# Kernel tuning notes

Measured on AMD Instinct MI355X. Metric: run time of the kernel, lower is better.

## Reference

```python
import jax, jax.numpy as jnp
import numpy as np

B, IN_CH, OUT_CH = 4, 64, 128
N_HIGH, N_LOW = 163842, 40962
GROUPS, EPS, SLOPE = 4, 1e-5, 0.2


def setup_inputs() -> dict:
    key = jax.random.key(0)
    ks = jax.random.split(key, 6)
    x = jax.random.normal(ks[0], (B, IN_CH, N_HIGH), jnp.float32)
    pool_neigh = jax.random.randint(ks[1], (N_LOW * 7,), 0, N_HIGH, dtype=jnp.int32)
    conv_neigh = jax.random.randint(ks[2], (N_LOW * 7,), 0, N_LOW, dtype=jnp.int32)
    W1 = jax.random.normal(ks[3], (OUT_CH, 7 * IN_CH), jnp.float32) / np.float32(np.sqrt(7 * IN_CH))
    b1 = jnp.zeros((OUT_CH,), jnp.float32)
    W2 = jax.random.normal(ks[4], (OUT_CH, 7 * OUT_CH), jnp.float32) / np.float32(np.sqrt(7 * OUT_CH))
    b2 = jnp.zeros((OUT_CH,), jnp.float32)
    return dict(x=x, pool_neigh=pool_neigh, conv_neigh=conv_neigh,
                W1=W1, b1=b1, gn1_w=jnp.ones((OUT_CH,), jnp.float32), gn1_b=jnp.zeros((OUT_CH,), jnp.float32),
                W2=W2, b2=b2, gn2_w=jnp.ones((OUT_CH,), jnp.float32), gn2_b=jnp.zeros((OUT_CH,), jnp.float32))


def _mean_pool(x, pool_neigh):
    # x: (B, C, N_high); pool_neigh: (N_low*7,) -> (B, C, N_low)
    g = x[:, :, pool_neigh].reshape(x.shape[0], x.shape[1], -1, 7)
    return g.mean(axis=-1)


def _onering_conv(x, neigh, W, b):
    # x: (B, C, N); neigh: (N*7,); W: (O, 7*C). Torch Linear over gathered
    # (N*7, C).view(N, 7*C): neighbor-major, channel-minor concatenation.
    Bb, C, N = x.shape
    feat = x[:, :, neigh].reshape(Bb, C, N, 7)            # (B, C, N, 7)
    feat = jnp.transpose(feat, (0, 2, 3, 1)).reshape(Bb, N, 7 * C)  # (B, N, 7C)
    out = jnp.einsum('bnf,of->bno', feat, W) + b          # (B, N, O)
    return jnp.transpose(out, (0, 2, 1))                  # (B, O, N)


def _group_norm(x, w, b):
    # x: (B, C, N), normalize per (group, sample) over (C//G, N)
    Bb, C, N = x.shape
    xg = x.reshape(Bb, GROUPS, C // GROUPS, N)
    mu = xg.mean(axis=(2, 3), keepdims=True)
    var = ((xg - mu) ** 2).mean(axis=(2, 3), keepdims=True)
    xn = ((xg - mu) * jax.lax.rsqrt(var + EPS)).reshape(Bb, C, N)
    return xn * w[None, :, None] + b[None, :, None]


def _leaky_relu(x):
    return jnp.where(x >= 0, x, SLOPE * x)


def reference(x, pool_neigh, conv_neigh, W1, b1, gn1_w, gn1_b, W2, b2, gn2_w, gn2_b):
    h = _mean_pool(x, pool_neigh)
    h = _leaky_relu(_group_norm(_onering_conv(h, conv_neigh, W1, b1), gn1_w, gn1_b))
    h = _leaky_relu(_group_norm(_onering_conv(h, conv_neigh, W2, b2), gn2_w, gn2_b))
    return h
```

## Files before the change

### kernel.cpp

```cpp
#include <hip/hip_runtime.h>

#define B_SZ 4
#define IN_CH 64
#define OUT_CH 128
#define NHI 163842
#define NLO 40962
#define EPS_GN 1e-5f
#define SLOPE 0.2f

typedef __attribute__((ext_vector_type(8))) short short8;
typedef __attribute__((ext_vector_type(16))) float f32x16;

__device__ inline ushort f2bf(float f) {
    union { float f; unsigned u; } v; v.f = f;
    unsigned r = v.u + 0x7FFF + ((v.u >> 16) & 1);
    return (ushort)(r >> 16);
}
__device__ inline float bf2f(ushort h) {
    union { unsigned u; float f; } v; v.u = ((unsigned)h) << 16;
    return v.f;
}

__device__ inline void glds16(const ushort* g, ushort* l) {
    typedef __attribute__((address_space(1))) const void gv;
    typedef __attribute__((address_space(3))) void lv;
    __builtin_amdgcn_global_load_lds((gv*)g, (lv*)l, 16, 0, 0);
}

__global__ void k_transpose_x(const float* __restrict__ x, ushort* __restrict__ xT) {
    __shared__ float t[64][65];
    const int b   = blockIdx.y;
    const int n0  = blockIdx.x * 64;
    const int tid = threadIdx.x;
    const int nq  = tid & 15;
    const int c0  = tid >> 4;
    const bool full = (n0 + 64) <= NHI;
    if (full) {
#pragma unroll
        for (int r = 0; r < 4; ++r) {
            int c = c0 + r * 16;
            float4 v = *(const float4*)&x[((long)b * IN_CH + c) * NHI + n0 + nq * 4];
            t[c][nq * 4 + 0] = v.x; t[c][nq * 4 + 1] = v.y;
            t[c][nq * 4 + 2] = v.z; t[c][nq * 4 + 3] = v.w;
        }
    } else {
        for (int r = 0; r < 4; ++r) {
            int c = c0 + r * 16;
            for (int e = 0; e < 4; ++e) {
                int n = n0 + nq * 4 + e;
                t[c][nq * 4 + e] = (n < NHI) ? x[((long)b * IN_CH + c) * NHI + n] : 0.f;
            }
        }
    }
    __syncthreads();
    const int n  = tid >> 2;
    const int cc = (tid & 3) * 16;
    if (n0 + n < NHI) {
        short8 o0, o1;
#pragma unroll
        for (int e = 0; e < 8; ++e) {
            o0[e] = (short)f2bf(t[cc + e][n]);
            o1[e] = (short)f2bf(t[cc + 8 + e][n]);
        }
        ushort* p = &xT[((long)b * NHI + n0 + n) * 64 + cc];
        *(short8*)p = o0;
        *(short8*)(p + 8) = o1;
    }
}

__global__ void k_prep_w(const float* __restrict__ W, ushort* __restrict__ Wb, int K) {
    int i = blockIdx.x * 256 + threadIdx.x;
    if (i >= K * 128) return;
    int k = i / 128, o = i % 128;
    int step = k >> 6, kk = k & 63, kg = kk >> 3, e = kk & 7;
    Wb[(((long)(step * 8 + kg) * 128 + o) * 8) + e] = f2bf(W[(long)o * K + k]);
}

__global__ void k_pool(const ushort* __restrict__ xT, const int* __restrict__ pn,
                       ushort* __restrict__ h1) {
    long t = (long)blockIdx.x * 256 + threadIdx.x;
    const long total = (long)B_SZ * NLO * 8;
    if (t >= total) return;
    int  cq = (int)(t & 7);
    long bn = t >> 3;
    int  n  = (int)(bn % NLO);
    int  b  = (int)(bn / NLO);
    float acc[8] = {};
#pragma unroll
    for (int j = 0; j < 7; ++j) {
        int idx = pn[n * 7 + j];
        short8 v = *(const short8*)&xT[((long)b * NHI + idx) * 64 + cq * 8];
#pragma unroll
        for (int e = 0; e < 8; ++e) acc[e] += bf2f((ushort)v[e]);
    }
    short8 o;
#pragma unroll
    for (int e = 0; e < 8; ++e) o[e] = (short)f2bf(acc[e] * (1.f / 7.f));
    *(short8*)&h1[bn * 64 + cq * 8] = o;
}

template <int CIN>
__global__ __launch_bounds__(256, 2)
void k_conv_mfma(const ushort* __restrict__ src, const int* __restrict__ nbr,
                 const ushort* __restrict__ Wb, const float* __restrict__ bias,
                 ushort* __restrict__ out, float* __restrict__ part) {
    constexpr int NSTEP = 7 * CIN / 64;
    __shared__ ushort Bsm[2][8192];
    __shared__ float  red[4][4][2];

    const int b     = blockIdx.y;
    const int n0    = blockIdx.x * 256;
    const int tid   = threadIdx.x;
    const int lane  = tid & 63;
    const int wid   = tid >> 6;
    const int l31   = lane & 31;
    const int khalf = lane >> 5;

    const int rr0 = min(n0 + wid * 64 + l31, NLO - 1);
    const int rr1 = min(n0 + wid * 64 + 32 + l31, NLO - 1);
    int nb0[7], nb1[7];
#pragma unroll
    for (int j = 0; j < 7; ++j) {
        nb0[j] = nbr[rr0 * 7 + j];
        nb1[j] = nbr[rr1 * 7 + j];
    }

    const long srcb = (long)b * NLO * CIN;
    const int  koff = khalf * 8;

    f32x16 acc[2][4] = {};
    short8 a[2][4], an[2][4];

#pragma unroll
    for (int i = 0; i < 4; ++i) {
        int off = (wid * 4 + i) * 512;
        glds16(&Wb[off + lane * 8], &Bsm[0][off]);
    }
    {
        const ushort* s0 = &src[srcb + (long)nb0[0] * CIN + koff];
        const ushort* s1 = &src[srcb + (long)nb1[0] * CIN + koff];
#pragma unroll
        for (int kh = 0; kh < 4; ++kh) {
            a[0][kh] = *(const short8*)(s0 + kh * 16);
            a[1][kh] = *(const short8*)(s1 + kh * 16);
        }
    }

#pragma unroll
    for (int step = 0; step < NSTEP; ++step) {
        const int cur = step & 1;
        __syncthreads();
        if (step + 1 < NSTEP) {
#pragma unroll
            for (int i = 0; i < 4; ++i) {
                int off = (wid * 4 + i) * 512;
                glds16(&Wb[(long)(step + 1) * 8192 + off + lane * 8], &Bsm[cur ^ 1][off]);
            }
            const int j2 = (CIN == 64) ? (step + 1) : ((step + 1) >> 1);
            const int cb2 = (CIN == 64) ? 0 : (((step + 1) & 1) * 64);
            const ushort* s0 = &src[srcb + (long)nb0[j2] * CIN + cb2 + koff];
            const ushort* s1 = &src[srcb + (long)nb1[j2] * CIN + cb2 + koff];
#pragma unroll
            for (int kh = 0; kh < 4; ++kh) {
                an[0][kh] = *(const short8*)(s0 + kh * 16);
                an[1][kh] = *(const short8*)(s1 + kh * 16);
            }
        }
#pragma unroll
        for (int kh = 0; kh < 4; ++kh) {
            const int kg = 2 * kh + khalf;
            const ushort* bb = &Bsm[cur][(kg * 128 + l31) * 8];
            short8 b0 = *(const short8*)(bb);
            short8 b1 = *(const short8*)(bb + 32 * 8);
            short8 b2 = *(const short8*)(bb + 64 * 8);
            short8 b3 = *(const short8*)(bb + 96 * 8);
            acc[0][0] = __builtin_amdgcn_mfma_f32_32x32x16_bf16(a[0][kh], b0, acc[0][0], 0, 0, 0);
            acc[0][1] = __builtin_amdgcn_mfma_f32_32x32x16_bf16(a[0][kh], b1, acc[0][1], 0, 0, 0);
            acc[0][2] = __builtin_amdgcn_mfma_f32_32x32x16_bf16(a[0][kh], b2, acc[0][2], 0, 0, 0);
            acc[0][3] = __builtin_amdgcn_mfma_f32_32x32x16_bf16(a[0][kh], b3, acc[0][3], 0, 0, 0);
            acc[1][0] = __builtin_amdgcn_mfma_f32_32x32x16_bf16(a[1][kh], b0, acc[1][0], 0, 0, 0);
            acc[1][1] = __builtin_amdgcn_mfma_f32_32x32x16_bf16(a[1][kh], b1, acc[1][1], 0, 0, 0);
            acc[1][2] = __builtin_amdgcn_mfma_f32_32x32x16_bf16(a[1][kh], b2, acc[1][2], 0, 0, 0);
            acc[1][3] = __builtin_amdgcn_mfma_f32_32x32x16_bf16(a[1][kh], b3, acc[1][3], 0, 0, 0);
        }
        if (step + 1 < NSTEP) {
#pragma unroll
            for (int kh = 0; kh < 4; ++kh) {
                a[0][kh] = an[0][kh];
                a[1][kh] = an[1][kh];
            }
        }
    }

    float bia[4];
#pragma unroll
    for (int n = 0; n < 4; ++n) bia[n] = bias[n * 32 + l31];
    float s[4] = {}, q[4] = {};
#pragma unroll
    for (int m = 0; m < 2; ++m)
#pragma unroll
        for (int n = 0; n < 4; ++n)
#pragma unroll
            for (int r = 0; r < 16; ++r) {
                int crow = (r & 3) + 8 * (r >> 2) + 4 * khalf;
                int row  = n0 + wid * 64 + m * 32 + crow;
                float v  = acc[m][n][r] + bia[n];
                if (row < NLO) {
                    out[((long)b * NLO + row) * 128 + n * 32 + l31] = f2bf(v);
                    s[n] += v; q[n] += v * v;
                }
            }
#pragma unroll
    for (int n = 0; n < 4; ++n)
#pragma unroll
        for (int off = 32; off > 0; off >>= 1) {
            s[n] += __shfl_down(s[n], off);
            q[n] += __shfl_down(q[n], off);
        }
    if (lane == 0) {
#pragma unroll
        for (int n = 0; n < 4; ++n) { red[wid][n][0] = s[n]; red[wid][n][1] = q[n]; }
    }
    __syncthreads();
    if (tid < 8) {
        int g = tid >> 1, isq = tid & 1;
        float v = red[0][g][isq] + red[1][g][isq] + red[2][g][isq] + red[3][g][isq];
        part[(((long)b * gridDim.x + blockIdx.x) * 4 + g) * 2 + isq] = v;
    }
}

__global__ void k_finalize(const float* __restrict__ part, int nblk,
                           const float* __restrict__ w, const float* __restrict__ bb,
                           float* __restrict__ scale, float* __restrict__ shift) {
    const int b = blockIdx.x >> 2, g = blockIdx.x & 3;
    const int tid = threadIdx.x;
    float s = 0.f, ss = 0.f;
    for (int k = tid; k < nblk; k += 256) {
        s  += part[(((long)b * nblk + k) * 4 + g) * 2 + 0];
        ss += part[(((long)b * nblk + k) * 4 + g) * 2 + 1];
    }
#pragma unroll
    for (int off = 32; off > 0; off >>= 1) {
        s += __shfl_down(s, off); ss += __shfl_down(ss, off);
    }
    __shared__ float red[8];
    __shared__ float fin[2];
    const int wave = tid >> 6, lane = tid & 63;
    if (lane == 0) { red[wave * 2] = s; red[wave * 2 + 1] = ss; }
    __syncthreads();
    if (tid == 0) {
        float as = red[0] + red[2] + red[4] + red[6];
        float aq = red[1] + red[3] + red[5] + red[7];
        const float cnt = 32.f * NLO;
        float mu  = as / cnt;
        float var = aq / cnt - mu * mu;
        fin[0] = mu; fin[1] = rsqrtf(var + EPS_GN);
    }
    __syncthreads();
    if (tid < 32) {
        int c = g * 32 + tid;
        float sc = fin[1] * w[c];
        scale[b * 128 + c] = sc;
        shift[b * 128 + c] = bb[c] - fin[0] * sc;
    }
}

__global__ void k_gnapply(const ushort* __restrict__ y, const float* __restrict__ sc,
                          const float* __restrict__ sh, ushort* __restrict__ yp) {
    long t = (long)blockIdx.x * 256 + threadIdx.x;
    const long total = (long)B_SZ * NLO * 16;
    if (t >= total) return;
    int  c8 = (int)(t & 15);
    long bn = t >> 4;
    int  b  = (int)(bn / NLO);
    short8 v = *(const short8*)&y[bn * 128 + c8 * 8];
    short8 o;
#pragma unroll
    for (int e = 0; e < 8; ++e) {
        int c = c8 * 8 + e;
        float f = bf2f((ushort)v[e]) * sc[b * 128 + c] + sh[b * 128 + c];
        f = fmaxf(f, SLOPE * f);
        o[e] = (short)f2bf(f);
    }
    *(short8*)&yp[bn * 128 + c8 * 8] = o;
}

__global__ void k_output(const ushort* __restrict__ y2, const float* __restrict__ scale,
                         const float* __restrict__ shift, float* __restrict__ out) {
    __shared__ float t[32][129];
    const int b   = blockIdx.y;
    const int n0  = blockIdx.x * 32;
    const int tid = threadIdx.x;
    const float* scb = &scale[b * 128];
    const float* shb = &shift[b * 128];
    const int c8 = (tid & 15) * 8;
#pragma unroll
    for (int r = 0; r < 2; ++r) {
        int nn = (tid >> 4) + r * 16;
        int n  = n0 + nn;
        if (n < NLO) {
            short8 v = *(const short8*)&y2[((long)b * NLO + n) * 128 + c8];
#pragma unroll
            for (int e = 0; e < 8; ++e) {
                int c = c8 + e;
                float f = bf2f((ushort)v[e]) * scb[c] + shb[c];
                t[nn][c] = fmaxf(f, SLOPE * f);
            }
        } else {
#pragma unroll
            for (int e = 0; e < 8; ++e) t[nn][c8 + e] = 0.f;
        }
    }
    __syncthreads();
    const int n4 = (tid & 7) * 4;
    const bool full = (n0 + 32) <= NLO;
#pragma unroll
    for (int r = 0; r < 4; ++r) {
        int c = (tid >> 3) + r * 32;
        long o = ((long)b * 128 + c) * NLO + n0 + n4;
        if (full) {
            float2 v0 = make_float2(t[n4][c], t[n4 + 1][c]);
            float2 v1 = make_float2(t[n4 + 2][c], t[n4 + 3][c]);
            *(float2*)&out[o]     = v0;
            *(float2*)&out[o + 2] = v1;
        } else {
            for (int e = 0; e < 4; ++e)
                if (n0 + n4 + e < NLO) out[o + e] = t[n4 + e][c];
        }
    }
}

extern "C" void kernel_launch(void* const* d_in, const int* in_sizes, int n_in,
                              void* d_out, int out_size, void* d_ws, size_t ws_size,
                              hipStream_t stream) {
    const float* x   = (const float*)d_in[0];
    const int*   pn  = (const int*)d_in[1];
    const int*   cn  = (const int*)d_in[2];
    const float* W1  = (const float*)d_in[3];
    const float* b1  = (const float*)d_in[4];
    const float* g1w = (const float*)d_in[5];
    const float* g1b = (const float*)d_in[6];
    const float* W2  = (const float*)d_in[7];
    const float* b2  = (const float*)d_in[8];
    const float* g2w = (const float*)d_in[9];
    const float* g2b = (const float*)d_in[10];
    float* out = (float*)d_out;
    char*  base = (char*)d_ws;

    ushort* xT  = (ushort*)(base + 0);
    ushort* y1  = (ushort*)(base + 0);
    ushort* y1p = (ushort*)(base + 44000000);
    ushort* h1  = (ushort*)(base + 88000000);
    ushort* y2  = (ushort*)(base + 110000000);
    ushort* wb1 = (ushort*)(base + 152000000);
    ushort* wb2 = (ushort*)(base + 152200000);
    float*  p1  = (float*)(base + 152500000);
    float*  p2  = (float*)(base + 152600000);
    float*  sc1 = (float*)(base + 152700000);
    float*  sh1 = sc1 + 512;
    float*  sc2 = (float*)(base + 152710000);
    float*  sh2 = sc2 + 512;

    const int NBLK = (NLO + 255) / 256;

    k_transpose_x<<<dim3((NHI + 63) / 64, B_SZ), 256, 0, stream>>>(x, xT);
    k_prep_w<<<(448 * 128 + 255) / 256, 256, 0, stream>>>(W1, wb1, 448);
    k_prep_w<<<(896 * 128 + 255) / 256, 256, 0, stream>>>(W2, wb2, 896);
    k_pool<<<(int)(((long)B_SZ * NLO * 8 + 255) / 256), 256, 0, stream>>>(xT, pn, h1);
    k_conv_mfma<64><<<dim3(NBLK, B_SZ), 256, 0, stream>>>(h1, cn, wb1, b1, y1, p1);
    k_finalize<<<16, 256, 0, stream>>>(p1, NBLK, g1w, g1b, sc1, sh1);
    k_gnapply<<<(int)(((long)B_SZ * NLO * 16 + 255) / 256), 256, 0, stream>>>(y1, sc1, sh1, y1p);
    k_conv_mfma<128><<<dim3(NBLK, B_SZ), 256, 0, stream>>>(y1p, cn, wb2, b2, y2, p2);
    k_finalize<<<16, 256, 0, stream>>>(p2, NBLK, g2w, g2b, sc2, sh2);
    k_output<<<dim3((NLO + 31) / 32, B_SZ), 256, 0, stream>>>(y2, sc2, sh2, out);
}
```

Before: 272.0 us.

## Retile conv MFMA kernel to 128-row blocks with LDS-staged gathered A tile

The one-ring conv kernel now processes 128 rows per block instead of 256, with the four waves arranged as a 2x2 grid over rows and output channels. The gathered neighbor features are loaded cooperatively and stored into a double-buffered LDS A tile before the MFMAs, instead of each wave loading its own rows straight into registers. This aims to make the gathers more contiguous, cut per-wave accumulator and register pressure, and double the number of blocks. In exchange it adds LDS write and read traffic, more LDS use per block, and a barrier every step. The GroupNorm partial-sum reduction is remapped to the new wave layout.

```diff
diff --git a/kernel.cpp b/kernel.cpp
--- a/kernel.cpp
+++ b/kernel.cpp
@@ -105,113 +105,109 @@
                  const ushort* __restrict__ Wb, const float* __restrict__ bias,
                  ushort* __restrict__ out, float* __restrict__ part) {
     constexpr int NSTEP = 7 * CIN / 64;
+    __shared__ ushort Asm[2][8192];
     __shared__ ushort Bsm[2][8192];
-    __shared__ float  red[4][4][2];
+    __shared__ float  red[4][2][2];
 
     const int b     = blockIdx.y;
-    const int n0    = blockIdx.x * 256;
+    const int n0    = blockIdx.x * 128;
     const int tid   = threadIdx.x;
     const int lane  = tid & 63;
-    const int wid   = tid >> 6;
+    const int wave  = tid >> 6;
+    const int wr    = wave >> 1, wc = wave & 1;
     const int l31   = lane & 31;
     const int khalf = lane >> 5;
 
-    const int rr0 = min(n0 + wid * 64 + l31, NLO - 1);
-    const int rr1 = min(n0 + wid * 64 + 32 + l31, NLO - 1);
+    const int s_nn = tid >> 2;
+    const int s_kq = tid & 3;
+    const int r0 = min(n0 + s_nn, NLO - 1);
+    const int r1 = min(n0 + 64 + s_nn, NLO - 1);
     int nb0[7], nb1[7];
 #pragma unroll
     for (int j = 0; j < 7; ++j) {
-        nb0[j] = nbr[rr0 * 7 + j];
-        nb1[j] = nbr[rr1 * 7 + j];
+        nb0[j] = nbr[r0 * 7 + j];
+        nb1[j] = nbr[r1 * 7 + j];
     }
 
     const long srcb = (long)b * NLO * CIN;
-    const int  koff = khalf * 8;
-
-    f32x16 acc[2][4] = {};
-    short8 a[2][4], an[2][4];
+    f32x16 acc[2][2] = {};
+    short8 a00, a01, a10, a11;
 
 #pragma unroll
     for (int i = 0; i < 4; ++i) {
-        int off = (wid * 4 + i) * 512;
+        int off = (wave * 4 + i) * 512;
         glds16(&Wb[off + lane * 8], &Bsm[0][off]);
     }
     {
-        const ushort* s0 = &src[srcb + (long)nb0[0] * CIN + koff];
-        const ushort* s1 = &src[srcb + (long)nb1[0] * CIN + koff];
-#pragma unroll
-        for (int kh = 0; kh < 4; ++kh) {
-            a[0][kh] = *(const short8*)(s0 + kh * 16);
-            a[1][kh] = *(const short8*)(s1 + kh * 16);
-        }
-    }
-
-#pragma unroll
+        const ushort* p0 = &src[srcb + (long)nb0[0] * CIN + s_kq * 8];
+        const ushort* p1 = &src[srcb + (long)nb1[0] * CIN + s_kq * 8];
+        a00 = *(const short8*)p0; a01 = *(const short8*)(p0 + 32);
+        a10 = *(const short8*)p1; a11 = *(const short8*)(p1 + 32);
+        *(short8*)&Asm[0][(s_kq * 128 + s_nn) * 8]            = a00;
+        *(short8*)&Asm[0][((s_kq + 4) * 128 + s_nn) * 8]      = a01;
+        *(short8*)&Asm[0][(s_kq * 128 + 64 + s_nn) * 8]       = a10;
+        *(short8*)&Asm[0][((s_kq + 4) * 128 + 64 + s_nn) * 8] = a11;
+    }
+    __syncthreads();
+
     for (int step = 0; step < NSTEP; ++step) {
         const int cur = step & 1;
-        __syncthreads();
+        const int nxt = cur ^ 1;
         if (step + 1 < NSTEP) {
 #pragma unroll
             for (int i = 0; i < 4; ++i) {
-                int off = (wid * 4 + i) * 512;
-                glds16(&Wb[(long)(step + 1) * 8192 + off + lane * 8], &Bsm[cur ^ 1][off]);
+                int off = (wave * 4 + i) * 512;
+                glds16(&Wb[(long)(step + 1) * 8192 + off + lane * 8], &Bsm[nxt][off]);
             }
-            const int j2 = (CIN == 64) ? (step + 1) : ((step + 1) >> 1);
-            const int cb2 = (CIN == 64) ? 0 : (((step + 1) & 1) * 64);
-            const ushort* s0 = &src[srcb + (long)nb0[j2] * CIN + cb2 + koff];
-            const ushort* s1 = &src[srcb + (long)nb1[j2] * CIN + cb2 + koff];
-#pragma unroll
-            for (int kh = 0; kh < 4; ++kh) {
-                an[0][kh] = *(const short8*)(s0 + kh * 16);
-                an[1][kh] = *(const short8*)(s1 + kh * 16);
-            }
+            const int s  = step + 1;
+            const int j  = (CIN == 64) ? s : (s >> 1);
+            const int cb = (CIN == 64) ? 0 : ((s & 1) * 64);
+            const ushort* p0 = &src[srcb + (long)nb0[j] * CIN + cb + s_kq * 8];
+            const ushort* p1 = &src[srcb + (long)nb1[j] * CIN + cb + s_kq * 8];
+            a00 = *(const short8*)p0; a01 = *(const short8*)(p0 + 32);
+            a10 = *(const short8*)p1; a11 = *(const short8*)(p1 + 32);
         }
 #pragma unroll
         for (int kh = 0; kh < 4; ++kh) {
             const int kg = 2 * kh + khalf;
-            const ushort* bb = &Bsm[cur][(kg * 128 + l31) * 8];
-            short8 b0 = *(const short8*)(bb);
-            short8 b1 = *(const short8*)(bb + 32 * 8);
-            short8 b2 = *(const short8*)(bb + 64 * 8);
-            short8 b3 = *(const short8*)(bb + 96 * 8);
-            acc[0][0] = __builtin_amdgcn_mfma_f32_32x32x16_bf16(a[0][kh], b0, acc[0][0], 0, 0, 0);
-            acc[0][1] = __builtin_amdgcn_mfma_f32_32x32x16_bf16(a[0][kh], b1, acc[0][1], 0, 0, 0);
-            acc[0][2] = __builtin_amdgcn_mfma_f32_32x32x16_bf16(a[0][kh], b2, acc[0][2], 0, 0, 0);
-            acc[0][3] = __builtin_amdgcn_mfma_f32_32x32x16_bf16(a[0][kh], b3, acc[0][3], 0, 0, 0);
-            acc[1][0] = __builtin_amdgcn_mfma_f32_32x32x16_bf16(a[1][kh], b0, acc[1][0], 0, 0, 0);
-            acc[1][1] = __builtin_amdgcn_mfma_f32_32x32x16_bf16(a[1][kh], b1, acc[1][1], 0, 0, 0);
-            acc[1][2] = __builtin_amdgcn_mfma_f32_32x32x16_bf16(a[1][kh], b2, acc[1][2], 0, 0, 0);
-            acc[1][3] = __builtin_amdgcn_mfma_f32_32x32x16_bf16(a[1][kh], b3, acc[1][3], 0, 0, 0);
+            short8 A0 = *(const short8*)&Asm[cur][(kg * 128 + wr * 64 + l31) * 8];
+            short8 A1 = *(const short8*)&Asm[cur][(kg * 128 + wr * 64 + 32 + l31) * 8];
+            short8 B0 = *(const short8*)&Bsm[cur][(kg * 128 + wc * 64 + l31) * 8];
+            short8 B1 = *(const short8*)&Bsm[cur][(kg * 128 + wc * 64 + 32 + l31) * 8];
+            acc[0][0] = __builtin_amdgcn_mfma_f32_32x32x16_bf16(A0, B0, acc[0][0], 0, 0, 0);
+            acc[0][1] = __builtin_amdgcn_mfma_f32_32x32x16_bf16(A0, B1, acc[0][1], 0, 0, 0);
+            acc[1][0] = __builtin_amdgcn_mfma_f32_32x32x16_bf16(A1, B0, acc[1][0], 0, 0, 0);
+            acc[1][1] = __builtin_amdgcn_mfma_f32_32x32x16_bf16(A1, B1, acc[1][1], 0, 0, 0);
         }
         if (step + 1 < NSTEP) {
-#pragma unroll
-            for (int kh = 0; kh < 4; ++kh) {
-                a[0][kh] = an[0][kh];
-                a[1][kh] = an[1][kh];
-            }
-        }
-    }
-
-    float bia[4];
-#pragma unroll
-    for (int n = 0; n < 4; ++n) bia[n] = bias[n * 32 + l31];
-    float s[4] = {}, q[4] = {};
+            *(short8*)&Asm[nxt][(s_kq * 128 + s_nn) * 8]            = a00;
+            *(short8*)&Asm[nxt][((s_kq + 4) * 128 + s_nn) * 8]      = a01;
+            *(short8*)&Asm[nxt][(s_kq * 128 + 64 + s_nn) * 8]       = a10;
+            *(short8*)&Asm[nxt][((s_kq + 4) * 128 + 64 + s_nn) * 8] = a11;
+        }
+        __syncthreads();
+    }
+
+    float bia[2];
+#pragma unroll
+    for (int n = 0; n < 2; ++n) bia[n] = bias[wc * 64 + n * 32 + l31];
+    float s[2] = {}, q[2] = {};
 #pragma unroll
     for (int m = 0; m < 2; ++m)
 #pragma unroll
-        for (int n = 0; n < 4; ++n)
+        for (int n = 0; n < 2; ++n)
 #pragma unroll
             for (int r = 0; r < 16; ++r) {
                 int crow = (r & 3) + 8 * (r >> 2) + 4 * khalf;
-                int row  = n0 + wid * 64 + m * 32 + crow;
+                int row  = n0 + wr * 64 + m * 32 + crow;
                 float v  = acc[m][n][r] + bia[n];
                 if (row < NLO) {
-                    out[((long)b * NLO + row) * 128 + n * 32 + l31] = f2bf(v);
+                    out[((long)b * NLO + row) * 128 + wc * 64 + n * 32 + l31] = f2bf(v);
                     s[n] += v; q[n] += v * v;
                 }
             }
 #pragma unroll
-    for (int n = 0; n < 4; ++n)
+    for (int n = 0; n < 2; ++n)
 #pragma unroll
         for (int off = 32; off > 0; off >>= 1) {
             s[n] += __shfl_down(s[n], off);
@@ -219,12 +215,13 @@
         }
     if (lane == 0) {
 #pragma unroll
-        for (int n = 0; n < 4; ++n) { red[wid][n][0] = s[n]; red[wid][n][1] = q[n]; }
+        for (int n = 0; n < 2; ++n) { red[wave][n][0] = s[n]; red[wave][n][1] = q[n]; }
     }
     __syncthreads();
     if (tid < 8) {
         int g = tid >> 1, isq = tid & 1;
-        float v = red[0][g][isq] + red[1][g][isq] + red[2][g][isq] + red[3][g][isq];
+        int gwc = g >> 1, gn = g & 1;
+        float v = red[gwc][gn][isq] + red[2 + gwc][gn][isq];
         part[(((long)b * gridDim.x + blockIdx.x) * 4 + g) * 2 + isq] = v;
     }
 }
@@ -361,7 +358,7 @@
     float*  sc2 = (float*)(base + 152710000);
     float*  sh2 = sc2 + 512;
 
-    const int NBLK = (NLO + 255) / 256;
+    const int NBLK = (NLO + 127) / 128;
 
     k_transpose_x<<<dim3((NHI + 63) / 64, B_SZ), 256, 0, stream>>>(x, xT);
     k_prep_w<<<(448 * 128 + 255) / 256, 256, 0, stream>>>(W1, wb1, 448);
```

New measurement: 276.6 us. About the same (+1.7%).
